# Kernel tuning notes

Measured on AMD Instinct MI355X. Metric: run time of the kernel, lower is better.

Reference implementation:

```python
import jax, jax.numpy as jnp
import numpy as np

TABLE_SIZE = 256
I16_MIN, I16_MAX = -32768.0, 32767.0
I8_MIN, I8_MAX = -128.0, 127.0
MAX_SOFTMAX_VALUE = 1.0
OUT_SCALE = MAX_SOFTMAX_VALUE * 2.0 / 255.0            # int8 output scale
EXP_OUT_SCALE = 2.0 / 65535.0                          # qint16 exp output scale
RECIP_OUT_SCALE = (1.0 / 0.1) * 2.0 / 65535.0          # qint16 reciprocal output scale
# (xmin, xmax, kind) in ascending x order; 'table' = 256-entry LUT, 'line' = linear fit
EXP_REGIONS = [(-40.0, -20.0, 'line'), (-20.0, -10.0, 'table'), (-10.0, 0.0, 'table'), (0.0, 1.0, 'line')]
RECIP_REGIONS = [(0.001, 0.1, 'line'), (0.1, 250.0, 'table'), (250.0, 500.0, 'table'), (500.0, 700.0, 'line')]


def _quant(y, out_scale, qmin, qmax):
    return jnp.clip(jnp.round(y / out_scale), qmin, qmax)


def _piecewise(x, func, regions, out_scale, qmin, qmax):
    """Piecewise quantized approximation of func: constant / line / 256-entry
    table regions, returning quantized (integer-valued float) outputs."""
    left_c = _quant(func(jnp.float32(regions[0][0])), out_scale, qmin, qmax)
    y = left_c * jnp.ones_like(x)
    for xmin, xmax, kind in regions:
        if kind == 'table':
            xs = jnp.linspace(xmin, xmax, TABLE_SIZE)
            tab = _quant(func(xs), out_scale, qmin, qmax)
            idx = jnp.clip(jnp.round((x - xmin) * ((TABLE_SIZE - 1) / (xmax - xmin))), 0, TABLE_SIZE - 1).astype(jnp.int32)
            y_r = tab[idx]
        else:
            y0 = func(jnp.float32(xmin))
            y1 = func(jnp.float32(xmax))
            y_r = _quant(y0 + (x - xmin) * ((y1 - y0) / (xmax - xmin)), out_scale, qmin, qmax)
        y = jnp.where(x >= xmin, y_r, y)
    right_c = _quant(func(jnp.float32(regions[-1][1])), out_scale, qmin, qmax)
    return jnp.where(x > regions[-1][1], right_c, y)


def setup_inputs() -> dict:
    key = jax.random.key(0)
    k1, _ = jax.random.split(key)
    data = jax.random.randint(k1, (32, 128, 80, 80), -128, 128, dtype=jnp.int32)  # int8 repr, zp=0
    data_scale = jnp.array([0.0625], dtype=jnp.float32)
    return {"data": data, "data_scale": data_scale}


def reference(data, data_scale):
    ds = data_scale[0]
    C = data.shape[1]
    shift = float(np.ceil(np.log2(C)))  # rescale_shift for the exp-sum
    # max-subtract in the integer domain, dequantize diff (zero_point = 0)
    qmax = jnp.max(data, axis=1, keepdims=True)
    xd = (data - qmax).astype(jnp.float32) * ds  # [B,C,H,W], in (-inf, 0]
    # quantized exp via piecewise tables -> qint16 with EXP_OUT_SCALE
    exp_q = _piecewise(xd, jnp.exp, EXP_REGIONS, EXP_OUT_SCALE, I16_MIN, I16_MAX)
    # sum over channels, right-shift back into int16 range
    sum_q = jnp.sum(exp_q, axis=1, keepdims=True)
    sum_sh = jnp.clip(jnp.round(sum_q * (2.0 ** -shift)), I16_MIN, I16_MAX)
    div_scale = EXP_OUT_SCALE * (2.0 ** shift)  # div_data_scale
    # quantized reciprocal of the (dequantized) shifted sum -> qint16
    recip_q = _piecewise(sum_sh * div_scale, lambda v: 1.0 / v, RECIP_REGIONS, RECIP_OUT_SCALE, I16_MIN, I16_MAX)
    # out = exp * recip, requantized to int8 with OUT_SCALE, then dequantized
    out_q = jnp.clip(jnp.round(exp_q * recip_q * (EXP_OUT_SCALE * RECIP_OUT_SCALE / OUT_SCALE)), I8_MIN, I8_MAX)
    return out_q * OUT_SCALE
```

## Files before the change

### kernel.cpp

```cpp
#include <hip/hip_runtime.h>
#include <cmath>

#define NB  32
#define NC  128
#define NHW 6400
#define PIX 64
#define TPB 256

typedef float vfloat4 __attribute__((ext_vector_type(4)));


__global__ __launch_bounds__(TPB) void qsoftmax_kernel(
    const int* __restrict__ data,
    const float* __restrict__ dscale,
    float* __restrict__ out) {
#pragma clang fp contract(off)
  __shared__ int   exp_tab[256];
  __shared__ float recip_tab[256];
  __shared__ int4  red_m[16][16];
  __shared__ int4  red_s[16][16];

  const int t  = threadIdx.x;
  const int k  = t >> 4;
  const int p4 = t & 15;

  const int blk  = blockIdx.x;
  const int b    = blk / (NHW / PIX);
  const int hw0  = (blk % (NHW / PIX)) * PIX;
  const int base4 = b * NC * (NHW / 4) + (hw0 >> 2);

  const float ds = dscale[0];

  {
    const float EXP_SCALE_F = (float)(2.0 / 65535.0);
    float x = (float)(-t) * ds;
    float e;
    if (x >= 0.0f) {
      float y0 = expf(0.0f), y1 = expf(1.0f);
      e = rintf((y0 + x * ((y1 - y0) / 1.0f)) / EXP_SCALE_F);
    } else if (x >= -10.0f) {
      float delta = 10.0f / 255.0f;
      float idxf = rintf((x + 10.0f) * 25.5f);
      idxf = fminf(fmaxf(idxf, 0.0f), 255.0f);
      float xs = -10.0f + idxf * delta;
      e = rintf((float)exp((double)xs) / EXP_SCALE_F);
    } else {
      float delta = 10.0f / 255.0f;
      float idxf = rintf((x + 20.0f) * 25.5f);
      idxf = fminf(fmaxf(idxf, 0.0f), 255.0f);
      float xs = -20.0f + idxf * delta;
      e = rintf((float)exp((double)xs) / EXP_SCALE_F);
    }
    e = fminf(fmaxf(e, -32768.0f), 32767.0f);
    exp_tab[t] = (int)e;

    const float RECIP_SCALE_F = (float)((1.0 / 0.1) * 2.0 / 65535.0);
    float deltar = (250.0f - 0.1f) / 255.0f;
    float xs = 0.1f + (float)t * deltar;
    float r = rintf((1.0f / xs) / RECIP_SCALE_F);
    r = fminf(fmaxf(r, -32768.0f), 32767.0f);
    recip_tab[t] = r;
  }

  const int4* g4 = (const int4*)data;
  int pd[8];
  int4 m = make_int4(-128, -128, -128, -128);
#pragma unroll
  for (int i = 0; i < 8; ++i) {
    int4 v = g4[base4 + (16 * i + k) * (NHW / 4) + p4];
    m.x = max(m.x, v.x); m.y = max(m.y, v.y);
    m.z = max(m.z, v.z); m.w = max(m.w, v.w);
    pd[i] = (v.x & 255) | ((v.y & 255) << 8) | ((v.z & 255) << 16) |
            (int)((unsigned)(v.w & 255) << 24);
  }
  red_m[k][p4] = m;
  __syncthreads();

  int4 q = red_m[0][p4];
#pragma unroll
  for (int kk = 1; kk < 16; ++kk) {
    int4 r = red_m[kk][p4];
    q.x = max(q.x, r.x); q.y = max(q.y, r.y);
    q.z = max(q.z, r.z); q.w = max(q.w, r.w);
  }

  int pe[16];
  int4 s = make_int4(0, 0, 0, 0);
#pragma unroll
  for (int i = 0; i < 8; ++i) {
    int pdv = pd[i];
    int c0 = (pdv << 24) >> 24;
    int c1 = (pdv << 16) >> 24;
    int c2 = (pdv << 8) >> 24;
    int c3 = pdv >> 24;
    int e0 = exp_tab[q.x - c0];
    int e1 = exp_tab[q.y - c1];
    int e2 = exp_tab[q.z - c2];
    int e3 = exp_tab[q.w - c3];
    s.x += e0; s.y += e1; s.z += e2; s.w += e3;
    pe[2 * i]     = e0 | (e1 << 16);
    pe[2 * i + 1] = e2 | (e3 << 16);
  }
  red_s[k][p4] = s;
  __syncthreads();

  int4 tot = red_s[0][p4];
#pragma unroll
  for (int kk = 1; kk < 16; ++kk) {
    int4 r = red_s[kk][p4];
    tot.x += r.x; tot.y += r.y; tot.z += r.z; tot.w += r.w;
  }
  const float DIV_SCALE_F = (float)((2.0 / 65535.0) * 128.0);
  const float RIDX_K_F    = (float)(255.0 / (250.0 - 0.1));
  float rq[4];
  {
    int tv[4] = {tot.x, tot.y, tot.z, tot.w};
#pragma unroll
    for (int j = 0; j < 4; ++j) {
      float ss = rintf((float)tv[j] * 0.0078125f);
      ss = fminf(fmaxf(ss, -32768.0f), 32767.0f);
      float v = ss * DIV_SCALE_F;
      float idxf = rintf((v - 0.1f) * RIDX_K_F);
      idxf = fminf(fmaxf(idxf, 0.0f), 255.0f);
      rq[j] = recip_tab[(int)idxf];
    }
  }

  const float K_F = (float)((2.0 / 65535.0) * ((1.0 / 0.1) * 2.0 / 65535.0) / (2.0 / 255.0));
  const float OUT_SCALE_F = (float)(2.0 / 255.0);
  vfloat4* o4 = (vfloat4*)out;
#pragma unroll
  for (int i = 0; i < 8; ++i) {
    int pa = pe[2 * i], pb = pe[2 * i + 1];
    float e0 = (float)(pa & 0xFFFF);
    float e1 = (float)(pa >> 16);
    float e2 = (float)(pb & 0xFFFF);
    float e3 = (float)(pb >> 16);
    vfloat4 o;
    o.x = fminf(fmaxf(rintf((e0 * rq[0]) * K_F), -128.0f), 127.0f) * OUT_SCALE_F;
    o.y = fminf(fmaxf(rintf((e1 * rq[1]) * K_F), -128.0f), 127.0f) * OUT_SCALE_F;
    o.z = fminf(fmaxf(rintf((e2 * rq[2]) * K_F), -128.0f), 127.0f) * OUT_SCALE_F;
    o.w = fminf(fmaxf(rintf((e3 * rq[3]) * K_F), -128.0f), 127.0f) * OUT_SCALE_F;
    __builtin_nontemporal_store(o, &o4[base4 + (16 * i + k) * (NHW / 4) + p4]);
  }
}

extern "C" void kernel_launch(void* const* d_in, const int* in_sizes, int n_in,
                              void* d_out, int out_size, void* d_ws, size_t ws_size,
                              hipStream_t stream) {
  const int* data     = (const int*)d_in[0];
  const float* dscale = (const float*)d_in[1];
  float* out          = (float*)d_out;
  (void)in_sizes; (void)n_in; (void)d_ws; (void)ws_size; (void)out_size;

  dim3 grid(NB * (NHW / PIX));
  qsoftmax_kernel<<<grid, TPB, 0, stream>>>(data, dscale, out);
}
```

Measured before the change: 185.9 us.

## Replace shared-memory channel reductions with wavefront shuffle reductions

Remaps threads so each wavefront covers all 128 channels for four pixel quads, letting the max and sum reductions over channels use xor shuffles instead of shared-memory staging and block barriers. This removes LDS traffic and one barrier, adding an explicit barrier after table setup. Global accesses become 64-byte contiguous segments per channel row instead of 256-byte ones, which may reduce coalescing efficiency.

```diff
diff --git a/kernel.cpp b/kernel.cpp
--- a/kernel.cpp
+++ b/kernel.cpp
@@ -17,17 +17,17 @@
 #pragma clang fp contract(off)
   __shared__ int   exp_tab[256];
   __shared__ float recip_tab[256];
-  __shared__ int4  red_m[16][16];
-  __shared__ int4  red_s[16][16];
 
-  const int t  = threadIdx.x;
-  const int k  = t >> 4;
-  const int p4 = t & 15;
+  const int t   = threadIdx.x;
+  const int l   = t & 63;
+  const int w   = t >> 6;
+  const int kq  = (l >> 2) & 15;
+  const int qw  = (w << 2) | (l & 3);
 
   const int blk  = blockIdx.x;
   const int b    = blk / (NHW / PIX);
   const int hw0  = (blk % (NHW / PIX)) * PIX;
-  const int base4 = b * NC * (NHW / 4) + (hw0 >> 2);
+  const int base4 = b * NC * (NHW / 4) + (hw0 >> 2) + qw;
 
   const float ds = dscale[0];
 
@@ -61,27 +61,26 @@
     r = fminf(fmaxf(r, -32768.0f), 32767.0f);
     recip_tab[t] = r;
   }
+  __syncthreads();
 
   const int4* g4 = (const int4*)data;
   int pd[8];
   int4 m = make_int4(-128, -128, -128, -128);
 #pragma unroll
   for (int i = 0; i < 8; ++i) {
-    int4 v = g4[base4 + (16 * i + k) * (NHW / 4) + p4];
+    int4 v = g4[base4 + (16 * i + kq) * (NHW / 4)];
     m.x = max(m.x, v.x); m.y = max(m.y, v.y);
     m.z = max(m.z, v.z); m.w = max(m.w, v.w);
     pd[i] = (v.x & 255) | ((v.y & 255) << 8) | ((v.z & 255) << 16) |
             (int)((unsigned)(v.w & 255) << 24);
   }
-  red_m[k][p4] = m;
-  __syncthreads();
 
-  int4 q = red_m[0][p4];
 #pragma unroll
-  for (int kk = 1; kk < 16; ++kk) {
-    int4 r = red_m[kk][p4];
-    q.x = max(q.x, r.x); q.y = max(q.y, r.y);
-    q.z = max(q.z, r.z); q.w = max(q.w, r.w);
+  for (int xm = 4; xm <= 32; xm <<= 1) {
+    m.x = max(m.x, __shfl_xor(m.x, xm, 64));
+    m.y = max(m.y, __shfl_xor(m.y, xm, 64));
+    m.z = max(m.z, __shfl_xor(m.z, xm, 64));
+    m.w = max(m.w, __shfl_xor(m.w, xm, 64));
   }
 
   int pe[16];
@@ -93,28 +92,28 @@
     int c1 = (pdv << 16) >> 24;
     int c2 = (pdv << 8) >> 24;
     int c3 = pdv >> 24;
-    int e0 = exp_tab[q.x - c0];
-    int e1 = exp_tab[q.y - c1];
-    int e2 = exp_tab[q.z - c2];
-    int e3 = exp_tab[q.w - c3];
+    int e0 = exp_tab[m.x - c0];
+    int e1 = exp_tab[m.y - c1];
+    int e2 = exp_tab[m.z - c2];
+    int e3 = exp_tab[m.w - c3];
     s.x += e0; s.y += e1; s.z += e2; s.w += e3;
     pe[2 * i]     = e0 | (e1 << 16);
     pe[2 * i + 1] = e2 | (e3 << 16);
   }
-  red_s[k][p4] = s;
-  __syncthreads();
 
-  int4 tot = red_s[0][p4];
 #pragma unroll
-  for (int kk = 1; kk < 16; ++kk) {
-    int4 r = red_s[kk][p4];
-    tot.x += r.x; tot.y += r.y; tot.z += r.z; tot.w += r.w;
+  for (int xm = 4; xm <= 32; xm <<= 1) {
+    s.x += __shfl_xor(s.x, xm, 64);
+    s.y += __shfl_xor(s.y, xm, 64);
+    s.z += __shfl_xor(s.z, xm, 64);
+    s.w += __shfl_xor(s.w, xm, 64);
   }
+
   const float DIV_SCALE_F = (float)((2.0 / 65535.0) * 128.0);
   const float RIDX_K_F    = (float)(255.0 / (250.0 - 0.1));
   float rq[4];
   {
-    int tv[4] = {tot.x, tot.y, tot.z, tot.w};
+    int tv[4] = {s.x, s.y, s.z, s.w};
 #pragma unroll
     for (int j = 0; j < 4; ++j) {
       float ss = rintf((float)tv[j] * 0.0078125f);
@@ -141,7 +140,7 @@
     o.y = fminf(fmaxf(rintf((e1 * rq[1]) * K_F), -128.0f), 127.0f) * OUT_SCALE_F;
     o.z = fminf(fmaxf(rintf((e2 * rq[2]) * K_F), -128.0f), 127.0f) * OUT_SCALE_F;
     o.w = fminf(fmaxf(rintf((e3 * rq[3]) * K_F), -128.0f), 127.0f) * OUT_SCALE_F;
-    __builtin_nontemporal_store(o, &o4[base4 + (16 * i + k) * (NHW / 4) + p4]);
+    __builtin_nontemporal_store(o, &o4[base4 + (16 * i + kq) * (NHW / 4)]);
   }
 }
 
```

Result: slower. 199.1 us (+7.1%).
